# Kernel tuning notes

Measured on AMD Instinct MI355X. Metric: run time of the kernel, lower is better.

The kernel has to match this reference:

```python
import jax, jax.numpy as jnp
import numpy as np
import math

B, C, H, W = 4, 256, 64, 64
N_GROUPS = 32
D_K = 64
N_HEADS = C // D_K  # 4
EPS = 1e-5


def setup_inputs() -> dict:
    key = jax.random.key(0)
    ks = jax.random.split(key, 7)
    return {
        "x": jax.random.normal(ks[0], (B, C, H, W), dtype=jnp.float32),
        "gamma": jax.random.uniform(ks[1], (C,), dtype=jnp.float32),
        "beta": jax.random.normal(ks[2], (C,), dtype=jnp.float32) * 0.1,
        "W_qkv": jax.random.normal(ks[3], (C, N_HEADS * D_K * 3), dtype=jnp.float32) * 0.02,
        "b_qkv": jax.random.normal(ks[4], (N_HEADS * D_K * 3,), dtype=jnp.float32) * 0.02,
        "W_out": jax.random.normal(ks[5], (N_HEADS * D_K, C), dtype=jnp.float32) * 0.02,
        "b_out": jax.random.normal(ks[6], (C,), dtype=jnp.float32) * 0.02,
    }


def _group_norm(x, gamma, beta):
    # x: [B, C, H, W], 32 groups, biased variance, eps=1e-5 (torch GroupNorm defaults)
    b, c, h, w = x.shape
    xg = x.reshape(b, N_GROUPS, c // N_GROUPS, h, w)
    mean = jnp.mean(xg, axis=(2, 3, 4), keepdims=True)
    var = jnp.var(xg, axis=(2, 3, 4), keepdims=True)
    xn = (xg - mean) / jnp.sqrt(var + EPS)
    xn = xn.reshape(b, c, h, w)
    return xn * gamma[None, :, None, None] + beta[None, :, None, None]


def reference(x, gamma, beta, W_qkv, b_qkv, W_out, b_out):
    b, c, h, w = x.shape
    n = h * w
    scale = 1.0 / math.sqrt(math.sqrt(D_K))
    # norm -> [B, N, C]
    hid = _group_norm(x, gamma, beta).reshape(b, c, n).transpose(0, 2, 1)
    # qkv projection -> [B, N, n_heads, 3*d_k], chunk on last dim
    qkv = (hid @ W_qkv + b_qkv).reshape(b, n, N_HEADS, 3 * D_K)
    q, k, v = jnp.split(qkv, 3, axis=-1)  # each [B, N, H, d_k]
    attn = jnp.einsum('bihd,bjhd->bijh', q * scale, k * scale)
    attn = jax.nn.softmax(attn, axis=2)  # softmax over j (keys)
    res = jnp.einsum('bijh,bjhd->bihd', attn, v).reshape(b, n, N_HEADS * D_K)
    res = res @ W_out + b_out  # [B, N, C]
    res = res.transpose(0, 2, 1).reshape(b, c, h, w)
    return (res + x) / math.sqrt(2.0)
```

## Files before the change

kernel.cpp:

```cpp
#include <hip/hip_runtime.h>
#include <math.h>

typedef float  f32x4  __attribute__((ext_vector_type(4)));
typedef __bf16 bf16x8 __attribute__((ext_vector_type(8)));
typedef __bf16 bf16x4 __attribute__((ext_vector_type(4)));

#define MFMA16(a, b, c) __builtin_amdgcn_mfma_f32_16x16x32_bf16((a), (b), (c), 0, 0, 0)

#define TRR(dst, a, lit)  asm volatile("ds_read_b64_tr_b16 %0, %1 offset:" lit : "=v"(dst) : "v"(a))
#define TRRM(dst, a, lit) asm volatile("ds_read_b64_tr_b16 %0, %1 offset:" lit : "=v"(dst) : "v"(a) : "memory")
#define SHUF8(a, b) __builtin_shufflevector((a), (b), 0, 1, 2, 3, 4, 5, 6, 7)

typedef __attribute__((address_space(3))) unsigned int lds_u32;
typedef __attribute__((address_space(1))) const unsigned int glb_u32;

__device__ __forceinline__ void gload16(const __bf16* g, char* l) {
    __builtin_amdgcn_global_load_lds((glb_u32*)g, (lds_u32*)l, 16, 0, 0);
}

static constexpr int BATCH = 4;
static constexpr int CH    = 256;
static constexpr int M_TOT = BATCH * 4096;

static constexpr float QSCALE = 0.18033688011112042f;

static constexpr size_t OFF_WQKV  = 0;
static constexpr size_t OFF_WOUT  = 196608ull * 2;
static constexpr size_t OFF_STATS = OFF_WOUT + 65536ull * 2;
static constexpr size_t OFF_HID   = OFF_STATS + 1024;
static constexpr size_t OFF_Q     = OFF_HID + (size_t)M_TOT * CH * 2;
static constexpr size_t OFF_K     = OFF_Q   + (size_t)M_TOT * CH * 2;
static constexpr size_t OFF_V     = OFF_K   + (size_t)M_TOT * CH * 2;

__global__ __launch_bounds__(256) void pre_kernel(const float* __restrict__ x,
                                                  float2* __restrict__ stats,
                                                  const float* __restrict__ wq,
                                                  const float* __restrict__ wo,
                                                  __bf16* __restrict__ wqf,
                                                  __bf16* __restrict__ wof) {
    if (blockIdx.x < 128) {
        int bg = blockIdx.x;
        const float4* p = (const float4*)(x + (size_t)bg * 32768);
        float s = 0.f, ss = 0.f;
        for (int i = threadIdx.x; i < 8192; i += 256) {
            float4 v = p[i];
            s  += (v.x + v.y) + (v.z + v.w);
            ss += v.x * v.x + v.y * v.y + v.z * v.z + v.w * v.w;
        }
#pragma unroll
        for (int d = 32; d > 0; d >>= 1) { s += __shfl_down(s, d); ss += __shfl_down(ss, d); }
        __shared__ float sh[8];
        int w = threadIdx.x >> 6, l = threadIdx.x & 63;
        if (l == 0) { sh[w] = s; sh[4 + w] = ss; }
        __syncthreads();
        if (threadIdx.x == 0) {
            float S = sh[0] + sh[1] + sh[2] + sh[3];
            float SS = sh[4] + sh[5] + sh[6] + sh[7];
            float mean = S * (1.f / 32768.f);
            float var  = SS * (1.f / 32768.f) - mean * mean;
            stats[bg] = make_float2(mean, rsqrtf(var + 1e-5f));
        }
    } else {
        int i = (blockIdx.x - 128) * 256 + threadIdx.x;
        if (i < 196608) {
            int e = i & 7, l = (i >> 3) & 63, kk = (i >> 9) & 7, jt = i >> 12;
            int kidx = kk * 32 + ((l >> 4) << 3) + e;
            int n = jt * 16 + (l & 15);
            wqf[i] = (__bf16)wq[kidx * 768 + n];
        } else {
            int i2 = i - 196608;
            int e = i2 & 7, l = (i2 >> 3) & 63, kk = (i2 >> 9) & 7, jt = i2 >> 12;
            int kidx = kk * 32 + ((l >> 4) << 3) + e;
            int n = jt * 16 + (l & 15);
            wof[i2] = (__bf16)wo[kidx * 256 + n];
        }
    }
}

__global__ __launch_bounds__(256) void gn_apply(const float* __restrict__ x,
                                                const float* __restrict__ gamma,
                                                const float* __restrict__ beta,
                                                const float2* __restrict__ stats,
                                                __bf16* __restrict__ hid) {
    int b  = blockIdx.x >> 6;
    int n0 = (blockIdx.x & 63) << 6;
    int c  = threadIdx.x;
    float2 st = stats[b * 32 + (c >> 3)];
    float gm = gamma[c] * st.y;
    float bt = beta[c] - st.x * gm;
    const float* xp = x + ((size_t)(b * 256 + c)) * 4096 + n0;
    __bf16* hp = hid + ((size_t)(b * 4096 + n0)) * 256 + c;
#pragma unroll
    for (int j4 = 0; j4 < 16; ++j4) {
        float4 v = *(const float4*)(xp + j4 * 4);
        hp[(size_t)(j4 * 4 + 0) * 256] = (__bf16)(v.x * gm + bt);
        hp[(size_t)(j4 * 4 + 1) * 256] = (__bf16)(v.y * gm + bt);
        hp[(size_t)(j4 * 4 + 2) * 256] = (__bf16)(v.z * gm + bt);
        hp[(size_t)(j4 * 4 + 3) * 256] = (__bf16)(v.w * gm + bt);
    }
}

__global__ __launch_bounds__(256) void qkv_gemm(const __bf16* __restrict__ hid,
                                                const __bf16* __restrict__ wf,
                                                const float* __restrict__ bqkv,
                                                __bf16* __restrict__ qb,
                                                __bf16* __restrict__ kb,
                                                __bf16* __restrict__ vb) {
    const int mt = blockIdx.x, nt = blockIdx.y;
    const int tid = threadIdx.x;
    const int w = tid >> 6, l = tid & 63;
    const int lr = l & 15, lh = l >> 4;
    f32x4 acc[4] = {{0.f,0.f,0.f,0.f},{0.f,0.f,0.f,0.f},{0.f,0.f,0.f,0.f},{0.f,0.f,0.f,0.f}};
    const __bf16* ap = hid + (size_t)(mt * 64 + w * 16 + lr) * 256 + lh * 8;
#pragma unroll
    for (int kk = 0; kk < 8; ++kk) {
        bf16x8 a = *(const bf16x8*)(ap + kk * 32);
#pragma unroll
        for (int fj = 0; fj < 4; ++fj) {
            bf16x8 bf = *(const bf16x8*)(wf + (size_t)(((nt * 4 + fj) * 8 + kk) * 64 + l) * 8);
            acc[fj] = MFMA16(a, bf, acc[fj]);
        }
    }
    int mbase = mt * 64 + w * 16 + lh * 4;
#pragma unroll
    for (int fj = 0; fj < 4; ++fj) {
        int j = nt * 64 + fj * 16 + lr;
        int head = j / 192, rem = j % 192;
        int part = rem >> 6, dd = rem & 63;
        float bias = bqkv[j];
        float sc = (part == 0) ? QSCALE : 1.0f;
        __bf16* dst = (part == 0) ? qb : (part == 1) ? kb : vb;
#pragma unroll
        for (int r = 0; r < 4; ++r) {
            int m = mbase + r;
            int b = m >> 12, n = m & 4095;
            dst[((size_t)((b * 4 + head) * 4096 + n)) * 64 + dd] = (__bf16)((acc[fj][r] + bias) * sc);
        }
    }
}

__global__ __launch_bounds__(256, 4) void attn_fwd(const __bf16* __restrict__ q,
                                                   const __bf16* __restrict__ k,
                                                   const __bf16* __restrict__ v,
                                                   __bf16* __restrict__ ao) {
    const int id = blockIdx.x;
    const int within = id >> 3;
    const int bh = ((id & 7) << 1) + (within >> 6);
    const int q0 = (within & 63) * 64;
    const int tid = threadIdx.x;
    const int wv = tid >> 6, l = tid & 63;
    const int lr = l & 15, lh = l >> 4;

    __shared__ __attribute__((aligned(16))) char smem[32768];

    const size_t base = (size_t)bh * (4096 * 64);

    const int c0 = wv * 64 + l;
    const int rK = c0 >> 3, cbK = l & 7;
    const int gk0 = rK * 64 + (cbK ^ (rK & 7)) * 8;
    const int gk1 = gk0 + 2048;
    const int dt0 = c0 >> 7, kq0 = (c0 >> 3) & 15, klo0 = (l >> 1) & 3, d80 = l & 1;
    const int gv0 = (kq0 * 4 + klo0) * 64 + dt0 * 16 + d80 * 8;
    const int gv1 = gv0 + 32;
    const int lw0 = wv * 1024;
    const int lw1 = 4096 + wv * 1024;

    const __bf16* kg = k + base;
    const __bf16* vg = v + base;

    const unsigned vA0 = (unsigned)(size_t)(smem + 16384) + (unsigned)(lr * 2 + lh * 128);
    const unsigned vA1 = vA0 + 8192u;

    bf16x8 qf0, qf1;
    {
        const __bf16* qp = q + base + (size_t)(q0 + wv * 16 + lr) * 64 + lh * 8;
        qf0 = *(const bf16x8*)qp;
        qf1 = *(const bf16x8*)(qp + 32);
    }
    bf16x8 ones;
#pragma unroll
    for (int e = 0; e < 8; ++e) ones[e] = (__bf16)1.0f;

    f32x4 o[4] = {{0.f,0.f,0.f,0.f},{0.f,0.f,0.f,0.f},{0.f,0.f,0.f,0.f},{0.f,0.f,0.f,0.f}};
    f32x4 o4 = {0.f, 0.f, 0.f, 0.f};

    gload16(kg + gk0, smem + lw0);
    gload16(kg + gk1, smem + lw1);
    gload16(vg + gv0, smem + 16384 + lw0);
    gload16(vg + gv1, smem + 16384 + lw1);
    __syncthreads();

    auto body = [&](const char* Kc, unsigned vA, char* kd, char* vd, int tnext) {
        if (tnext < 64) {
            const __bf16* kp = kg + (size_t)tnext * 4096;
            const __bf16* vp = vg + (size_t)tnext * 4096;
            gload16(kp + gk0, kd + lw0);
            gload16(kp + gk1, kd + lw1);
            gload16(vp + gv0, vd + lw0);
            gload16(vp + gv1, vd + lw1);
        }

        f32x4 s[4];
        const f32x4 z = {0.f, 0.f, 0.f, 0.f};
        __builtin_amdgcn_s_setprio(1);
#pragma unroll
        for (int fj = 0; fj < 4; ++fj) {
            int row = fj * 16 + lr;
            bf16x8 kb0 = *(const bf16x8*)(Kc + row * 128 + ((lh * 16) ^ ((row & 7) << 4)));
            bf16x8 kb1 = *(const bf16x8*)(Kc + row * 128 + (((4 + lh) * 16) ^ ((row & 7) << 4)));
            s[fj] = MFMA16(kb0, qf0, z);
            s[fj] = MFMA16(kb1, qf1, s[fj]);
        }
        __builtin_amdgcn_s_setprio(0);

        bf16x4 u0, u1, u2, u3, u4, u5, u6, u7, u8, u9, u10, u11, u12, u13, u14, u15;
        TRRM(u0,  vA, "0");    TRR(u1,  vA, "512");
        TRR(u2,  vA, "1024");  TRR(u3,  vA, "1536");
        TRR(u4,  vA, "2048");  TRR(u5,  vA, "2560");
        TRR(u6,  vA, "3072");  TRR(u7,  vA, "3584");
        TRR(u8,  vA, "4096");  TRR(u9,  vA, "4608");
        TRR(u10, vA, "5120");  TRR(u11, vA, "5632");
        TRR(u12, vA, "6144");  TRR(u13, vA, "6656");
        TRR(u14, vA, "7168");  TRR(u15, vA, "7680");

        bf16x8 B0, B1;
#pragma unroll
        for (int fj = 0; fj < 4; ++fj)
#pragma unroll
            for (int r = 0; r < 4; ++r) {
                float pp = __builtin_amdgcn_exp2f(s[fj][r]);
                if (fj < 2) B0[fj * 4 + r] = (__bf16)pp;
                else        B1[(fj - 2) * 4 + r] = (__bf16)pp;
            }

        asm volatile("s_waitcnt lgkmcnt(0)" ::: "memory");
        __builtin_amdgcn_sched_barrier(0);
        __builtin_amdgcn_s_setprio(1);
        o4   = MFMA16(ones, B0, o4);
        o[0] = MFMA16(SHUF8(u0,  u1),  B0, o[0]);
        o[0] = MFMA16(SHUF8(u2,  u3),  B1, o[0]);
        o[1] = MFMA16(SHUF8(u4,  u5),  B0, o[1]);
        o[1] = MFMA16(SHUF8(u6,  u7),  B1, o[1]);
        o4   = MFMA16(ones, B1, o4);
        o[2] = MFMA16(SHUF8(u8,  u9),  B0, o[2]);
        o[2] = MFMA16(SHUF8(u10, u11), B1, o[2]);
        o[3] = MFMA16(SHUF8(u12, u13), B0, o[3]);
        o[3] = MFMA16(SHUF8(u14, u15), B1, o[3]);
        __builtin_amdgcn_s_setprio(0);

        __syncthreads();
    };

    for (int t = 0; t < 64; t += 2) {
        body(smem,        vA0, smem + 8192, smem + 16384 + 8192, t + 1);
        body(smem + 8192, vA1, smem,        smem + 16384,        t + 2);
    }

    float inv = 1.0f / o4[0];
    int b = bh >> 2, h = bh & 3;
    int n = q0 + wv * 16 + lr;
    __bf16* dst = ao + ((size_t)(b * 4096 + n)) * 256 + h * 64 + lh * 4;
#pragma unroll
    for (int fd = 0; fd < 4; ++fd) {
        bf16x4 pk;
#pragma unroll
        for (int r = 0; r < 4; ++r) pk[r] = (__bf16)(o[fd][r] * inv);
        *(bf16x4*)(dst + fd * 16) = pk;
    }
}

__global__ __launch_bounds__(256) void out_gemm(const __bf16* __restrict__ ao,
                                                const __bf16* __restrict__ wf,
                                                const float* __restrict__ bout,
                                                const float* __restrict__ x,
                                                float* __restrict__ out) {
    const int mt = blockIdx.x, nt = blockIdx.y;
    const int tid = threadIdx.x;
    const int w = tid >> 6, l = tid & 63;
    const int lr = l & 15, lh = l >> 4;
    f32x4 acc[4] = {{0.f,0.f,0.f,0.f},{0.f,0.f,0.f,0.f},{0.f,0.f,0.f,0.f},{0.f,0.f,0.f,0.f}};
    const __bf16* ap = ao + (size_t)(mt * 64 + w * 16 + lr) * 256 + lh * 8;
#pragma unroll
    for (int kk = 0; kk < 8; ++kk) {
        bf16x8 a = *(const bf16x8*)(ap + kk * 32);
#pragma unroll
        for (int fj = 0; fj < 4; ++fj) {
            bf16x8 bf = *(const bf16x8*)(wf + (size_t)(((nt * 4 + fj) * 8 + kk) * 64 + l) * 8);
            acc[fj] = MFMA16(a, bf, acc[fj]);
        }
    }
    __shared__ float tile[64][72];
#pragma unroll
    for (int fj = 0; fj < 4; ++fj) {
        float bias = bout[nt * 64 + fj * 16 + lr];
#pragma unroll
        for (int r = 0; r < 4; ++r)
            tile[w * 16 + lh * 4 + r][fj * 16 + lr] = acc[fj][r] + bias;
    }
    __syncthreads();
    int b  = mt >> 6;
    int n0 = (mt & 63) * 64;
    int c0 = nt * 64;
    int cl = tid >> 2, nq = tid & 3;
    size_t gbase = ((size_t)(b * 256 + c0 + cl)) * 4096 + n0 + nq * 16;
#pragma unroll
    for (int i = 0; i < 16; i += 4) {
        float4 xv = *(const float4*)(x + gbase + i);
        float4 ov;
        ov.x = (tile[nq * 16 + i + 0][cl] + xv.x) * 0.70710678118654752f;
        ov.y = (tile[nq * 16 + i + 1][cl] + xv.y) * 0.70710678118654752f;
        ov.z = (tile[nq * 16 + i + 2][cl] + xv.z) * 0.70710678118654752f;
        ov.w = (tile[nq * 16 + i + 3][cl] + xv.w) * 0.70710678118654752f;
        *(float4*)(out + gbase + i) = ov;
    }
}

extern "C" void kernel_launch(void* const* d_in, const int* in_sizes, int n_in,
                              void* d_out, int out_size, void* d_ws, size_t ws_size,
                              hipStream_t stream) {
    const float* x     = (const float*)d_in[0];
    const float* gamma = (const float*)d_in[1];
    const float* beta  = (const float*)d_in[2];
    const float* W_qkv = (const float*)d_in[3];
    const float* b_qkv = (const float*)d_in[4];
    const float* W_out = (const float*)d_in[5];
    const float* b_out = (const float*)d_in[6];
    float* out = (float*)d_out;
    char* ws = (char*)d_ws;

    __bf16* wqf   = (__bf16*)(ws + OFF_WQKV);
    __bf16* wof   = (__bf16*)(ws + OFF_WOUT);
    float2* stats = (float2*)(ws + OFF_STATS);
    __bf16* hid   = (__bf16*)(ws + OFF_HID);
    __bf16* qb    = (__bf16*)(ws + OFF_Q);
    __bf16* kb    = (__bf16*)(ws + OFF_K);
    __bf16* vb    = (__bf16*)(ws + OFF_V);

    pre_kernel<<<1152, 256, 0, stream>>>(x, stats, W_qkv, W_out, wqf, wof);
    gn_apply<<<256, 256, 0, stream>>>(x, gamma, beta, stats, hid);
    qkv_gemm<<<dim3(256, 12), 256, 0, stream>>>(hid, wqf, b_qkv, qb, kb, vb);
    attn_fwd<<<1024, 256, 0, stream>>>(qb, kb, vb, hid);
    out_gemm<<<dim3(256, 4), 256, 0, stream>>>(hid, wof, b_out, x, out);
}
```

Baseline: 144.4 us.

## Process two query tiles per attention block to reuse K/V loads

```diff
diff --git a/kernel.cpp b/kernel.cpp
--- a/kernel.cpp
+++ b/kernel.cpp
@@ -139,14 +139,14 @@
     }
 }
 
-__global__ __launch_bounds__(256, 4) void attn_fwd(const __bf16* __restrict__ q,
+__global__ __launch_bounds__(256, 2) void attn_fwd(const __bf16* __restrict__ q,
                                                    const __bf16* __restrict__ k,
                                                    const __bf16* __restrict__ v,
                                                    __bf16* __restrict__ ao) {
     const int id = blockIdx.x;
     const int within = id >> 3;
-    const int bh = ((id & 7) << 1) + (within >> 6);
-    const int q0 = (within & 63) * 64;
+    const int bh = ((id & 7) << 1) + (within >> 5);
+    const int q0 = (within & 31) * 128;
     const int tid = threadIdx.x;
     const int wv = tid >> 6, l = tid & 63;
     const int lr = l & 15, lh = l >> 4;
@@ -171,18 +171,22 @@
     const unsigned vA0 = (unsigned)(size_t)(smem + 16384) + (unsigned)(lr * 2 + lh * 128);
     const unsigned vA1 = vA0 + 8192u;
 
-    bf16x8 qf0, qf1;
+    bf16x8 qf0a, qf1a, qf0b, qf1b;
     {
         const __bf16* qp = q + base + (size_t)(q0 + wv * 16 + lr) * 64 + lh * 8;
-        qf0 = *(const bf16x8*)qp;
-        qf1 = *(const bf16x8*)(qp + 32);
+        qf0a = *(const bf16x8*)qp;
+        qf1a = *(const bf16x8*)(qp + 32);
+        qf0b = *(const bf16x8*)(qp + 4096);
+        qf1b = *(const bf16x8*)(qp + 4096 + 32);
     }
     bf16x8 ones;
 #pragma unroll
     for (int e = 0; e < 8; ++e) ones[e] = (__bf16)1.0f;
 
-    f32x4 o[4] = {{0.f,0.f,0.f,0.f},{0.f,0.f,0.f,0.f},{0.f,0.f,0.f,0.f},{0.f,0.f,0.f,0.f}};
-    f32x4 o4 = {0.f, 0.f, 0.f, 0.f};
+    f32x4 oa[4] = {{0.f,0.f,0.f,0.f},{0.f,0.f,0.f,0.f},{0.f,0.f,0.f,0.f},{0.f,0.f,0.f,0.f}};
+    f32x4 ob[4] = {{0.f,0.f,0.f,0.f},{0.f,0.f,0.f,0.f},{0.f,0.f,0.f,0.f},{0.f,0.f,0.f,0.f}};
+    f32x4 o4a = {0.f, 0.f, 0.f, 0.f};
+    f32x4 o4b = {0.f, 0.f, 0.f, 0.f};
 
     gload16(kg + gk0, smem + lw0);
     gload16(kg + gk1, smem + lw1);
@@ -200,7 +204,7 @@
             gload16(vp + gv1, vd + lw1);
         }
 
-        f32x4 s[4];
+        f32x4 sa[4], sb[4];
         const f32x4 z = {0.f, 0.f, 0.f, 0.f};
         __builtin_amdgcn_s_setprio(1);
 #pragma unroll
@@ -208,8 +212,10 @@
             int row = fj * 16 + lr;
             bf16x8 kb0 = *(const bf16x8*)(Kc + row * 128 + ((lh * 16) ^ ((row & 7) << 4)));
             bf16x8 kb1 = *(const bf16x8*)(Kc + row * 128 + (((4 + lh) * 16) ^ ((row & 7) << 4)));
-            s[fj] = MFMA16(kb0, qf0, z);
-            s[fj] = MFMA16(kb1, qf1, s[fj]);
+            sa[fj] = MFMA16(kb0, qf0a, z);
+            sb[fj] = MFMA16(kb0, qf0b, z);
+            sa[fj] = MFMA16(kb1, qf1a, sa[fj]);
+            sb[fj] = MFMA16(kb1, qf1b, sb[fj]);
         }
         __builtin_amdgcn_s_setprio(0);
 
@@ -223,29 +229,34 @@
         TRR(u12, vA, "6144");  TRR(u13, vA, "6656");
         TRR(u14, vA, "7168");  TRR(u15, vA, "7680");
 
-        bf16x8 B0, B1;
+        bf16x8 Ba0, Ba1, Bb0, Bb1;
 #pragma unroll
         for (int fj = 0; fj < 4; ++fj)
 #pragma unroll
             for (int r = 0; r < 4; ++r) {
-                float pp = __builtin_amdgcn_exp2f(s[fj][r]);
-                if (fj < 2) B0[fj * 4 + r] = (__bf16)pp;
-                else        B1[(fj - 2) * 4 + r] = (__bf16)pp;
+                float pa = __builtin_amdgcn_exp2f(sa[fj][r]);
+                float pb = __builtin_amdgcn_exp2f(sb[fj][r]);
+                if (fj < 2) { Ba0[fj * 4 + r] = (__bf16)pa; Bb0[fj * 4 + r] = (__bf16)pb; }
+                else        { Ba1[(fj - 2) * 4 + r] = (__bf16)pa; Bb1[(fj - 2) * 4 + r] = (__bf16)pb; }
             }
 
         asm volatile("s_waitcnt lgkmcnt(0)" ::: "memory");
         __builtin_amdgcn_sched_barrier(0);
         __builtin_amdgcn_s_setprio(1);
-        o4   = MFMA16(ones, B0, o4);
-        o[0] = MFMA16(SHUF8(u0,  u1),  B0, o[0]);
-        o[0] = MFMA16(SHUF8(u2,  u3),  B1, o[0]);
-        o[1] = MFMA16(SHUF8(u4,  u5),  B0, o[1]);
-        o[1] = MFMA16(SHUF8(u6,  u7),  B1, o[1]);
-        o4   = MFMA16(ones, B1, o4);
-        o[2] = MFMA16(SHUF8(u8,  u9),  B0, o[2]);
-        o[2] = MFMA16(SHUF8(u10, u11), B1, o[2]);
-        o[3] = MFMA16(SHUF8(u12, u13), B0, o[3]);
-        o[3] = MFMA16(SHUF8(u14, u15), B1, o[3]);
+        bf16x8 v01 = SHUF8(u0,  u1),  v23 = SHUF8(u2,  u3);
+        bf16x8 v45 = SHUF8(u4,  u5),  v67 = SHUF8(u6,  u7);
+        oa[0] = MFMA16(v01, Ba0, oa[0]);  ob[0] = MFMA16(v01, Bb0, ob[0]);
+        oa[0] = MFMA16(v23, Ba1, oa[0]);  ob[0] = MFMA16(v23, Bb1, ob[0]);
+        oa[1] = MFMA16(v45, Ba0, oa[1]);  ob[1] = MFMA16(v45, Bb0, ob[1]);
+        oa[1] = MFMA16(v67, Ba1, oa[1]);  ob[1] = MFMA16(v67, Bb1, ob[1]);
+        o4a   = MFMA16(ones, Ba0, o4a);   o4b   = MFMA16(ones, Bb0, o4b);
+        bf16x8 v89 = SHUF8(u8,  u9),  vab = SHUF8(u10, u11);
+        bf16x8 vcd = SHUF8(u12, u13), vef = SHUF8(u14, u15);
+        oa[2] = MFMA16(v89, Ba0, oa[2]);  ob[2] = MFMA16(v89, Bb0, ob[2]);
+        oa[2] = MFMA16(vab, Ba1, oa[2]);  ob[2] = MFMA16(vab, Bb1, ob[2]);
+        oa[3] = MFMA16(vcd, Ba0, oa[3]);  ob[3] = MFMA16(vcd, Bb0, ob[3]);
+        oa[3] = MFMA16(vef, Ba1, oa[3]);  ob[3] = MFMA16(vef, Bb1, ob[3]);
+        o4a   = MFMA16(ones, Ba1, o4a);   o4b   = MFMA16(ones, Bb1, o4b);
         __builtin_amdgcn_s_setprio(0);
 
         __syncthreads();
@@ -256,16 +267,22 @@
         body(smem + 8192, vA1, smem,        smem + 16384,        t + 2);
     }
 
-    float inv = 1.0f / o4[0];
+    float inva = 1.0f / o4a[0];
+    float invb = 1.0f / o4b[0];
     int b = bh >> 2, h = bh & 3;
     int n = q0 + wv * 16 + lr;
-    __bf16* dst = ao + ((size_t)(b * 4096 + n)) * 256 + h * 64 + lh * 4;
+    __bf16* dsta = ao + ((size_t)(b * 4096 + n)) * 256 + h * 64 + lh * 4;
+    __bf16* dstb = dsta + 64 * 256;
 #pragma unroll
     for (int fd = 0; fd < 4; ++fd) {
-        bf16x4 pk;
-#pragma unroll
-        for (int r = 0; r < 4; ++r) pk[r] = (__bf16)(o[fd][r] * inv);
-        *(bf16x4*)(dst + fd * 16) = pk;
+        bf16x4 pka, pkb;
+#pragma unroll
+        for (int r = 0; r < 4; ++r) {
+            pka[r] = (__bf16)(oa[fd][r] * inva);
+            pkb[r] = (__bf16)(ob[fd][r] * invb);
+        }
+        *(bf16x4*)(dsta + fd * 16) = pka;
+        *(bf16x4*)(dstb + fd * 16) = pkb;
     }
 }
 
@@ -339,6 +356,6 @@
     pre_kernel<<<1152, 256, 0, stream>>>(x, stats, W_qkv, W_out, wqf, wof);
     gn_apply<<<256, 256, 0, stream>>>(x, gamma, beta, stats, hid);
     qkv_gemm<<<dim3(256, 12), 256, 0, stream>>>(hid, wqf, b_qkv, qb, kb, vb);
-    attn_fwd<<<1024, 256, 0, stream>>>(qb, kb, vb, hid);
+    attn_fwd<<<512, 256, 0, stream>>>(qb, kb, vb, hid);
     out_gemm<<<dim3(256, 4), 256, 0, stream>>>(hid, wof, b_out, x, out);
 }
```

Result: faster. 137.5 us (-4.8%).

## Switch attention kernel to 32x32x16 MFMA with 128-query tiles per block

Applied to the files above, without the earlier changes.

```diff
diff --git a/kernel.cpp b/kernel.cpp
--- a/kernel.cpp
+++ b/kernel.cpp
@@ -1,11 +1,13 @@
 #include <hip/hip_runtime.h>
 #include <math.h>
 
-typedef float  f32x4  __attribute__((ext_vector_type(4)));
-typedef __bf16 bf16x8 __attribute__((ext_vector_type(8)));
-typedef __bf16 bf16x4 __attribute__((ext_vector_type(4)));
+typedef float  f32x4   __attribute__((ext_vector_type(4)));
+typedef float  f32x16  __attribute__((ext_vector_type(16)));
+typedef __bf16 bf16x8  __attribute__((ext_vector_type(8)));
+typedef __bf16 bf16x4  __attribute__((ext_vector_type(4)));
 
 #define MFMA16(a, b, c) __builtin_amdgcn_mfma_f32_16x16x32_bf16((a), (b), (c), 0, 0, 0)
+#define MFMA32(a, b, c) __builtin_amdgcn_mfma_f32_32x32x16_bf16((a), (b), (c), 0, 0, 0)
 
 #define TRR(dst, a, lit)  asm volatile("ds_read_b64_tr_b16 %0, %1 offset:" lit : "=v"(dst) : "v"(a))
 #define TRRM(dst, a, lit) asm volatile("ds_read_b64_tr_b16 %0, %1 offset:" lit : "=v"(dst) : "v"(a) : "memory")
@@ -139,17 +141,17 @@
     }
 }
 
-__global__ __launch_bounds__(256, 4) void attn_fwd(const __bf16* __restrict__ q,
+__global__ __launch_bounds__(256, 2) void attn_fwd(const __bf16* __restrict__ q,
                                                    const __bf16* __restrict__ k,
                                                    const __bf16* __restrict__ v,
                                                    __bf16* __restrict__ ao) {
     const int id = blockIdx.x;
     const int within = id >> 3;
-    const int bh = ((id & 7) << 1) + (within >> 6);
-    const int q0 = (within & 63) * 64;
+    const int bh = ((id & 7) << 1) + (within >> 5);
+    const int q0 = (within & 31) * 128;
     const int tid = threadIdx.x;
     const int wv = tid >> 6, l = tid & 63;
-    const int lr = l & 15, lh = l >> 4;
+    const int l31 = l & 31, h = l >> 5;
 
     __shared__ __attribute__((aligned(16))) char smem[32768];
 
@@ -159,30 +161,45 @@
     const int rK = c0 >> 3, cbK = l & 7;
     const int gk0 = rK * 64 + (cbK ^ (rK & 7)) * 8;
     const int gk1 = gk0 + 2048;
-    const int dt0 = c0 >> 7, kq0 = (c0 >> 3) & 15, klo0 = (l >> 1) & 3, d80 = l & 1;
-    const int gv0 = (kq0 * 4 + klo0) * 64 + dt0 * 16 + d80 * 8;
-    const int gv1 = gv0 + 32;
+    auto vsrc = [](int c) -> int {
+        int u = c >> 5, r6 = (c >> 3) & 3, j = (c >> 1) & 3, d8 = c & 1;
+        int kstep = u >> 2, dt = (u >> 1) & 1, eh = u & 1;
+        int kt = kstep >> 1, s = kstep & 1;
+        int hq = r6 >> 1, hh = r6 & 1, e = eh * 4 + j;
+        int key = kt * 32 + s * 16 + (e >> 2) * 8 + hq * 4 + (e & 3);
+        return key * 64 + dt * 32 + hh * 16 + d8 * 8;
+    };
+    const int gv0 = vsrc(c0), gv1 = vsrc(c0 + 256);
     const int lw0 = wv * 1024;
     const int lw1 = 4096 + wv * 1024;
 
     const __bf16* kg = k + base;
     const __bf16* vg = v + base;
 
-    const unsigned vA0 = (unsigned)(size_t)(smem + 16384) + (unsigned)(lr * 2 + lh * 128);
+    const unsigned lanep = (unsigned)((l & 15) * 2 + (l >> 4) * 128);
+    const unsigned vA0 = (unsigned)(size_t)(smem + 16384) + lanep;
     const unsigned vA1 = vA0 + 8192u;
 
-    bf16x8 qf0, qf1;
+    int koff[2][4];
+#pragma unroll
+    for (int kt = 0; kt < 2; ++kt) {
+        int row = kt * 32 + l31;
+#pragma unroll
+        for (int ks = 0; ks < 4; ++ks)
+            koff[kt][ks] = row * 128 + ((ks * 32 + h * 16) ^ ((row & 7) << 4));
+    }
+
+    bf16x8 qf[4];
     {
-        const __bf16* qp = q + base + (size_t)(q0 + wv * 16 + lr) * 64 + lh * 8;
-        qf0 = *(const bf16x8*)qp;
-        qf1 = *(const bf16x8*)(qp + 32);
+        const __bf16* qp = q + base + (size_t)(q0 + wv * 32 + l31) * 64 + h * 8;
+#pragma unroll
+        for (int ks = 0; ks < 4; ++ks) qf[ks] = *(const bf16x8*)(qp + ks * 16);
     }
     bf16x8 ones;
 #pragma unroll
     for (int e = 0; e < 8; ++e) ones[e] = (__bf16)1.0f;
 
-    f32x4 o[4] = {{0.f,0.f,0.f,0.f},{0.f,0.f,0.f,0.f},{0.f,0.f,0.f,0.f},{0.f,0.f,0.f,0.f}};
-    f32x4 o4 = {0.f, 0.f, 0.f, 0.f};
+    f32x16 O0 = (f32x16)0.0f, O1 = (f32x16)0.0f, LS = (f32x16)0.0f;
 
     gload16(kg + gk0, smem + lw0);
     gload16(kg + gk1, smem + lw1);
@@ -200,16 +217,14 @@
             gload16(vp + gv1, vd + lw1);
         }
 
-        f32x4 s[4];
-        const f32x4 z = {0.f, 0.f, 0.f, 0.f};
+        f32x16 S0 = (f32x16)0.0f, S1 = (f32x16)0.0f;
         __builtin_amdgcn_s_setprio(1);
 #pragma unroll
-        for (int fj = 0; fj < 4; ++fj) {
-            int row = fj * 16 + lr;
-            bf16x8 kb0 = *(const bf16x8*)(Kc + row * 128 + ((lh * 16) ^ ((row & 7) << 4)));
-            bf16x8 kb1 = *(const bf16x8*)(Kc + row * 128 + (((4 + lh) * 16) ^ ((row & 7) << 4)));
-            s[fj] = MFMA16(kb0, qf0, z);
-            s[fj] = MFMA16(kb1, qf1, s[fj]);
+        for (int ks = 0; ks < 4; ++ks) {
+            bf16x8 ka0 = *(const bf16x8*)(Kc + koff[0][ks]);
+            bf16x8 ka1 = *(const bf16x8*)(Kc + koff[1][ks]);
+            S0 = MFMA32(ka0, qf[ks], S0);
+            S1 = MFMA32(ka1, qf[ks], S1);
         }
         __builtin_amdgcn_s_setprio(0);
 
@@ -223,29 +238,30 @@
         TRR(u12, vA, "6144");  TRR(u13, vA, "6656");
         TRR(u14, vA, "7168");  TRR(u15, vA, "7680");
 
-        bf16x8 B0, B1;
-#pragma unroll
-        for (int fj = 0; fj < 4; ++fj)
-#pragma unroll
-            for (int r = 0; r < 4; ++r) {
-                float pp = __builtin_amdgcn_exp2f(s[fj][r]);
-                if (fj < 2) B0[fj * 4 + r] = (__bf16)pp;
-                else        B1[(fj - 2) * 4 + r] = (__bf16)pp;
-            }
+        bf16x8 B0, B1, B2, B3;
+#pragma unroll
+        for (int e = 0; e < 8; ++e) {
+            B0[e] = (__bf16)__builtin_amdgcn_exp2f(S0[e]);
+            B1[e] = (__bf16)__builtin_amdgcn_exp2f(S0[8 + e]);
+            B2[e] = (__bf16)__builtin_amdgcn_exp2f(S1[e]);
+            B3[e] = (__bf16)__builtin_amdgcn_exp2f(S1[8 + e]);
+        }
 
         asm volatile("s_waitcnt lgkmcnt(0)" ::: "memory");
         __builtin_amdgcn_sched_barrier(0);
         __builtin_amdgcn_s_setprio(1);
-        o4   = MFMA16(ones, B0, o4);
-        o[0] = MFMA16(SHUF8(u0,  u1),  B0, o[0]);
-        o[0] = MFMA16(SHUF8(u2,  u3),  B1, o[0]);
-        o[1] = MFMA16(SHUF8(u4,  u5),  B0, o[1]);
-        o[1] = MFMA16(SHUF8(u6,  u7),  B1, o[1]);
-        o4   = MFMA16(ones, B1, o4);
-        o[2] = MFMA16(SHUF8(u8,  u9),  B0, o[2]);
-        o[2] = MFMA16(SHUF8(u10, u11), B1, o[2]);
-        o[3] = MFMA16(SHUF8(u12, u13), B0, o[3]);
-        o[3] = MFMA16(SHUF8(u14, u15), B1, o[3]);
+        O0 = MFMA32(SHUF8(u0,  u1),  B0, O0);
+        O1 = MFMA32(SHUF8(u2,  u3),  B0, O1);
+        LS = MFMA32(ones, B0, LS);
+        O0 = MFMA32(SHUF8(u4,  u5),  B1, O0);
+        O1 = MFMA32(SHUF8(u6,  u7),  B1, O1);
+        LS = MFMA32(ones, B1, LS);
+        O0 = MFMA32(SHUF8(u8,  u9),  B2, O0);
+        O1 = MFMA32(SHUF8(u10, u11), B2, O1);
+        LS = MFMA32(ones, B2, LS);
+        O0 = MFMA32(SHUF8(u12, u13), B3, O0);
+        O1 = MFMA32(SHUF8(u14, u15), B3, O1);
+        LS = MFMA32(ones, B3, LS);
         __builtin_amdgcn_s_setprio(0);
 
         __syncthreads();
@@ -256,16 +272,20 @@
         body(smem + 8192, vA1, smem,        smem + 16384,        t + 2);
     }
 
-    float inv = 1.0f / o4[0];
-    int b = bh >> 2, h = bh & 3;
-    int n = q0 + wv * 16 + lr;
-    __bf16* dst = ao + ((size_t)(b * 4096 + n)) * 256 + h * 64 + lh * 4;
-#pragma unroll
-    for (int fd = 0; fd < 4; ++fd) {
-        bf16x4 pk;
-#pragma unroll
-        for (int r = 0; r < 4; ++r) pk[r] = (__bf16)(o[fd][r] * inv);
-        *(bf16x4*)(dst + fd * 16) = pk;
+    float inv = 1.0f / LS[0];
+    int b = bh >> 2, hd = bh & 3;
+    int n = q0 + wv * 32 + l31;
+    __bf16* dst = ao + ((size_t)(b * 4096 + n)) * 256 + hd * 64 + h * 4;
+#pragma unroll
+    for (int dt = 0; dt < 2; ++dt) {
+        const f32x16& O = dt ? O1 : O0;
+#pragma unroll
+        for (int g = 0; g < 4; ++g) {
+            bf16x4 pk;
+#pragma unroll
+            for (int m = 0; m < 4; ++m) pk[m] = (__bf16)(O[g * 4 + m] * inv);
+            *(bf16x4*)(dst + dt * 32 + g * 8) = pk;
+        }
     }
 }
 
@@ -339,6 +359,6 @@
     pre_kernel<<<1152, 256, 0, stream>>>(x, stats, W_qkv, W_out, wqf, wof);
     gn_apply<<<256, 256, 0, stream>>>(x, gamma, beta, stats, hid);
     qkv_gemm<<<dim3(256, 12), 256, 0, stream>>>(hid, wqf, b_qkv, qb, kb, vb);
-    attn_fwd<<<1024, 256, 0, stream>>>(qb, kb, vb, hid);
+    attn_fwd<<<512, 256, 0, stream>>>(qb, kb, vb, hid);
     out_gemm<<<dim3(256, 4), 256, 0, stream>>>(hid, wof, b_out, x, out);
 }
```

Measured after the change: 143.7 us. No clear change (-0.5%).
